# Performance work log

Hardware: AMD Instinct MI355X
Metric: run time of the kernel (lower is better)

## Reference

```python
import jax, jax.numpy as jnp
import numpy as np

DT = 1.0
V_LAMBDA = 1e-4
V_RIDGE = 1e-4


def third_order_D(Np):
    # [Np-3, Np] banded third-difference operator
    M = Np - 3
    r = jnp.arange(M)
    D = jnp.zeros((M, Np), dtype=jnp.float32)
    D = D.at[r, r].set(-1.0).at[r, r + 1].set(3.0).at[r, r + 2].set(-3.0).at[r, r + 3].set(1.0)
    return D


def setup_inputs() -> dict:
    key = jax.random.key(0)
    k1, k2, k3 = jax.random.split(key, 3)
    B, N = 8192, 64
    dxy = jax.random.normal(k1, (B, N, 2), dtype=jnp.float32)
    theta = jax.random.normal(k2, (B, N + 1), dtype=jnp.float32)
    v0 = jax.random.normal(k3, (B,), dtype=jnp.float32)
    return {"dxy": dxy, "theta": theta, "v0": v0}


def reference(dxy, theta, v0):
    B, N, _ = dxy.shape  # theta: [B, N+1]
    g = (2.0 / DT) * dxy                     # [B, N, 2]
    b = g.reshape(B, 2 * N)                  # interleaved (x, y) per step
    cos_t = jnp.cos(theta)
    sin_t = jnp.sin(theta)

    # Assemble banded data matrix A: [B, 2N, N+1]
    rows = jnp.arange(N)
    A = jnp.zeros((B, 2 * N, N + 1), dtype=dxy.dtype)
    A = A.at[:, 2 * rows, rows].set(cos_t[:, :-1])
    A = A.at[:, 2 * rows, rows + 1].set(cos_t[:, 1:])
    A = A.at[:, 2 * rows + 1, rows].set(sin_t[:, :-1])
    A = A.at[:, 2 * rows + 1, rows + 1].set(sin_t[:, 1:])
    # data weights w = 1 -> Aw == A

    ATA = jnp.einsum('bij,bik->bjk', A, A)           # [B, N+1, N+1]
    rhs = jnp.einsum('bij,bi->bj', A[:, :, 1:], b)   # [B, N]
    rhs = rhs - ATA[:, 1:, 0] * v0[:, None]

    # Smoothness prior: third-order difference, lam3 = v_lambda / dt^6
    D3 = third_order_D(N + 1)
    DTD = (V_LAMBDA / DT ** 6) * (D3.T @ D3)         # [N+1, N+1], shared across batch
    rhs = rhs - DTD[1:, 0] * v0[:, None]

    lhs = ATA[:, 1:, 1:] + DTD[1:, 1:] + V_RIDGE * jnp.eye(N, dtype=dxy.dtype)
    L = jnp.linalg.cholesky(lhs)
    y = jax.scipy.linalg.cho_solve((L, True), rhs[..., None])[..., 0]  # [B, N]
    return jnp.concatenate([v0[:, None], y], axis=-1)                  # [B, N+1]
```

## Files before the change

kernel.cpp:

```cpp
#include <hip/hip_runtime.h>
#include <math.h>

#define LAM3  1e-4f
#define RIDGE 1e-4f
#define NN    64
#define NP    65

__device__ __forceinline__ float d3_diag(int f) {
    if (f == 0 || f == 64) return 1.f;
    if (f == 1 || f == 63) return 10.f;
    if (f == 2 || f == 62) return 19.f;
    return 20.f;
}
__device__ __forceinline__ float d3_off1(int f) {
    if (f == 1 || f == 64) return -3.f;
    if (f == 2 || f == 63) return -12.f;
    return -15.f;
}
__device__ __forceinline__ float d3_off2(int f) {
    if (f == 2 || f == 64) return 3.f;
    return 6.f;
}

__global__ __launch_bounds__(64, 1) void alpamayo_banded_solve(
    const float* __restrict__ dxy,
    const float* __restrict__ theta,
    const float* __restrict__ v0,
    float* __restrict__ out,
    int B)
{
    __shared__ float thS[64 * NP];
    __shared__ float dxS[64 * 130];

    const int tid = threadIdx.x;
    const long b0 = (long)blockIdx.x * 64;
    const int b = (int)b0 + tid;

    {
        const float4* g = (const float4*)(theta + b0 * NP);
        float4* s4 = (float4*)thS;
        const long lim = (long)B * NP - b0 * NP;
        #pragma unroll
        for (int it = 0; it < 17; ++it) {
            const int k = it * 64 + tid;
            if (k < 1040 && 4 * k + 3 < lim) s4[k] = g[k];
        }
    }
    {
        const float4* g = (const float4*)(dxy + b0 * 2 * NN);
        const long lim4 = ((long)B * 2 * NN - b0 * 2 * NN) / 4;
        #pragma unroll
        for (int it = 0; it < 32; ++it) {
            const int k = it * 64 + tid;
            if (k < lim4) {
                const float4 q = g[k];
                const int flat = 4 * k;
                const int addr = flat + 2 * (flat >> 7);
                dxS[addr + 0] = q.x; dxS[addr + 1] = q.y;
                dxS[addr + 2] = q.z; dxS[addr + 3] = q.w;
            }
        }
    }
    const float v0b = (b < B) ? v0[b] : 0.f;
    __syncthreads();

    if (b < B) {
        const float* thL = thS + tid * NP;
        const float* dxL = dxS + tid * 130;

        float L1a[NN], L2a[NN], L3a[NN], rda[NN], z[NN];

        float sp, cp;
        __sincosf(thL[0], &sp, &cp);
        float bxp = dxL[0], byp = dxL[1];

        float p1L1 = 0.f, p1L2 = 0.f, p2L1 = 0.f;
        float rd1 = 0.f, rd2 = 0.f, rd3 = 0.f;
        float z1 = 0.f, z2 = 0.f, z3 = 0.f;

        #pragma unroll
        for (int i = 0; i < NN; ++i) {
            const int f = i + 1;
            float sf, cf;
            __sincosf(thL[f], &sf, &cf);
            const float e = cp * cf + sp * sf;

            float bxc = 0.f, byc = 0.f;
            if (f < NN) { bxc = dxL[2 * f]; byc = dxL[2 * f + 1]; }
            float rhs = 2.f * (cf * (bxp + bxc) + sf * (byp + byc));

            if (i == 0) rhs -= (e + LAM3 * -3.f) * v0b;
            if (i == 1) rhs -= (LAM3 *  3.f) * v0b;
            if (i == 2) rhs -= (LAM3 * -1.f) * v0b;

            const float a0 = (f == NN ? 1.f : 2.f) + LAM3 * d3_diag(f) + RIDGE;
            const float a1 = e + LAM3 * d3_off1(f);
            const float a2 = LAM3 * d3_off2(f);
            const float a3 = LAM3 * -1.f;

            const float Li3 = a3 * rd3;
            const float Li2 = (a2 - Li3 * p2L1) * rd2;
            const float Li1 = (a1 - Li3 * p1L2 - Li2 * p1L1) * rd1;
            const float dg  = a0 - Li3 * Li3 - Li2 * Li2 - Li1 * Li1;
            const float rd0 = __builtin_amdgcn_rsqf(dg);

            const float zi = (rhs - Li3 * z3 - Li2 * z2 - Li1 * z1) * rd0;

            L1a[i] = Li1; L2a[i] = Li2; L3a[i] = Li3; rda[i] = rd0; z[i] = zi;

            p2L1 = p1L1; p1L1 = Li1; p1L2 = Li2;
            rd3 = rd2; rd2 = rd1; rd1 = rd0;
            z3 = z2; z2 = z1; z1 = zi;
            cp = cf; sp = sf; bxp = bxc; byp = byc;
        }

        float* yL = thS + tid * NP;
        float y1 = 0.f, y2 = 0.f, y3 = 0.f;
        #pragma unroll
        for (int i = NN - 1; i >= 0; --i) {
            float yi = z[i];
            if (i + 1 < NN) yi -= L1a[i + 1] * y1;
            if (i + 2 < NN) yi -= L2a[i + 2] * y2;
            if (i + 3 < NN) yi -= L3a[i + 3] * y3;
            yi *= rda[i];
            yL[1 + i] = yi;
            y3 = y2; y2 = y1; y1 = yi;
        }
        yL[0] = v0b;
    }
    __syncthreads();

    {
        float4* g = (float4*)(out + b0 * NP);
        const float4* s4 = (const float4*)thS;
        const long lim = (long)B * NP - b0 * NP;
        #pragma unroll
        for (int it = 0; it < 17; ++it) {
            const int k = it * 64 + tid;
            if (k < 1040 && 4 * k + 3 < lim) g[k] = s4[k];
        }
    }
}

extern "C" void kernel_launch(void* const* d_in, const int* in_sizes, int n_in,
                              void* d_out, int out_size, void* d_ws, size_t ws_size,
                              hipStream_t stream) {
    const float* dxy   = (const float*)d_in[0];
    const float* theta = (const float*)d_in[1];
    const float* v0    = (const float*)d_in[2];
    float* out = (float*)d_out;
    const int B = in_sizes[2];
    const int blocks = (B + 63) / 64;
    alpamayo_banded_solve<<<blocks, 64, 0, stream>>>(dxy, theta, v0, out, B);
}
```

Before: 78.49 us.

## Split banded solve into parallel prep kernel and sequential Cholesky kernel

Splits the single kernel in two. A 256-thread prep kernel computes sin/cos, the off-diagonal terms and the right-hand side in parallel across four threads per batch row, and writes them to workspace in a transposed layout. A 64-thread solve kernel then reads these with coalesced loads and runs only the serial Cholesky recurrence. This takes the trig and data-shuffling work off the serial critical path of each thread, at the cost of an extra launch and a round trip of 2*64*B floats through global memory. Bounds checks for a partial last block are removed, so it assumes B is a multiple of 64.

```diff
diff --git a/kernel.cpp b/kernel.cpp
--- a/kernel.cpp
+++ b/kernel.cpp
@@ -22,123 +22,151 @@
     return 6.f;
 }
 
-__global__ __launch_bounds__(64, 1) void alpamayo_banded_solve(
+__global__ __launch_bounds__(256, 1) void alpamayo_prep(
     const float* __restrict__ dxy,
     const float* __restrict__ theta,
+    const float* __restrict__ v0,
+    float* __restrict__ eT,
+    float* __restrict__ rT,
+    int B)
+{
+    __shared__ __attribute__((aligned(16))) float thS[64 * NP];
+    __shared__ float cS[64 * NP];
+    __shared__ float sS[64 * NP];
+    __shared__ float bxS[64 * NP];
+    __shared__ float byS[64 * NP];
+
+    const int tid = threadIdx.x;
+    const int b0 = blockIdx.x * 64;
+
+    {
+        const float4* g = (const float4*)(theta + (long)b0 * NP);
+        float4* s4 = (float4*)thS;
+        #pragma unroll
+        for (int it = 0; it < 5; ++it) {
+            const int k = it * 256 + tid;
+            if (k < 1040) s4[k] = g[k];
+        }
+    }
+    {
+        const float4* g = (const float4*)(dxy + (long)b0 * 128);
+        #pragma unroll
+        for (int it = 0; it < 8; ++it) {
+            const int k = it * 256 + tid;
+            const float4 q = g[k];
+            const int flat = 4 * k;
+            const int bl = flat >> 7;
+            const int i  = (flat & 127) >> 1;
+            float* bx = bxS + bl * NP + i;
+            float* by = byS + bl * NP + i;
+            bx[0] = q.x; by[0] = q.y; bx[1] = q.z; by[1] = q.w;
+        }
+    }
+    if (tid < 64) { bxS[tid * NP + 64] = 0.f; byS[tid * NP + 64] = 0.f; }
+    __syncthreads();
+
+    #pragma unroll
+    for (int it = 0; it < 17; ++it) {
+        const int k = it * 256 + tid;
+        if (k < 4160) {
+            float sv, cv;
+            __sincosf(thS[k], &sv, &cv);
+            sS[k] = sv; cS[k] = cv;
+        }
+    }
+    __syncthreads();
+
+    const int bl = tid & 63;
+    const int qr = tid >> 6;
+    const int b  = b0 + bl;
+    const float* cL  = cS  + bl * NP;
+    const float* sL  = sS  + bl * NP;
+    const float* bxL = bxS + bl * NP;
+    const float* byL = byS + bl * NP;
+    const float v0b = v0[b];
+
+    #pragma unroll
+    for (int p = 0; p < 16; ++p) {
+        const int i = p * 4 + qr;
+        const int f = i + 1;
+        const float e   = cL[i] * cL[f] + sL[i] * sL[f];
+        float rhs = 2.f * (cL[f] * (bxL[i] + bxL[f]) + sL[f] * (byL[i] + byL[f]));
+        if (i == 0) rhs -= (e + LAM3 * -3.f) * v0b;
+        if (i == 1) rhs -= (LAM3 *  3.f) * v0b;
+        if (i == 2) rhs -= (LAM3 * -1.f) * v0b;
+        eT[i * B + b] = e;
+        rT[i * B + b] = rhs;
+    }
+}
+
+__global__ __launch_bounds__(64, 1) void alpamayo_solve(
+    const float* __restrict__ eT,
+    const float* __restrict__ rT,
     const float* __restrict__ v0,
     float* __restrict__ out,
     int B)
 {
-    __shared__ float thS[64 * NP];
-    __shared__ float dxS[64 * 130];
+    __shared__ __attribute__((aligned(16))) float yS[64 * NP];
 
     const int tid = threadIdx.x;
-    const long b0 = (long)blockIdx.x * 64;
-    const int b = (int)b0 + tid;
+    const int b0 = blockIdx.x * 64;
+    const int b  = b0 + tid;
 
-    {
-        const float4* g = (const float4*)(theta + b0 * NP);
-        float4* s4 = (float4*)thS;
-        const long lim = (long)B * NP - b0 * NP;
-        #pragma unroll
-        for (int it = 0; it < 17; ++it) {
-            const int k = it * 64 + tid;
-            if (k < 1040 && 4 * k + 3 < lim) s4[k] = g[k];
-        }
+    float L1a[NN], L2a[NN], L3a[NN], rda[NN], z[NN];
+
+    float p1L1 = 0.f, p1L2 = 0.f, p2L1 = 0.f;
+    float rd1 = 0.f, rd2 = 0.f, rd3 = 0.f;
+    float z1 = 0.f, z2 = 0.f, z3 = 0.f;
+
+    const float* ep = eT + b;
+    const float* rp = rT + b;
+
+    #pragma unroll
+    for (int i = 0; i < NN; ++i) {
+        const int f = i + 1;
+        const float e   = ep[i * B];
+        const float rhs = rp[i * B];
+
+        const float a0 = (f == NN ? 1.f : 2.f) + LAM3 * d3_diag(f) + RIDGE;
+        const float a1 = e + LAM3 * d3_off1(f);
+        const float a2 = LAM3 * d3_off2(f);
+        const float a3 = LAM3 * -1.f;
+
+        const float Li3 = a3 * rd3;
+        const float Li2 = (a2 - Li3 * p2L1) * rd2;
+        const float Li1 = (a1 - Li3 * p1L2 - Li2 * p1L1) * rd1;
+        const float dg  = a0 - Li3 * Li3 - Li2 * Li2 - Li1 * Li1;
+        const float rd0 = __builtin_amdgcn_rsqf(dg);
+        const float zi  = (rhs - Li3 * z3 - Li2 * z2 - Li1 * z1) * rd0;
+
+        L1a[i] = Li1; L2a[i] = Li2; L3a[i] = Li3; rda[i] = rd0; z[i] = zi;
+
+        p2L1 = p1L1; p1L1 = Li1; p1L2 = Li2;
+        rd3 = rd2; rd2 = rd1; rd1 = rd0;
+        z3 = z2; z2 = z1; z1 = zi;
     }
-    {
-        const float4* g = (const float4*)(dxy + b0 * 2 * NN);
-        const long lim4 = ((long)B * 2 * NN - b0 * 2 * NN) / 4;
-        #pragma unroll
-        for (int it = 0; it < 32; ++it) {
-            const int k = it * 64 + tid;
-            if (k < lim4) {
-                const float4 q = g[k];
-                const int flat = 4 * k;
-                const int addr = flat + 2 * (flat >> 7);
-                dxS[addr + 0] = q.x; dxS[addr + 1] = q.y;
-                dxS[addr + 2] = q.z; dxS[addr + 3] = q.w;
-            }
-        }
+
+    float* yL = yS + tid * NP;
+    float y1 = 0.f, y2 = 0.f, y3 = 0.f;
+    #pragma unroll
+    for (int i = NN - 1; i >= 0; --i) {
+        float yi = z[i];
+        if (i + 1 < NN) yi -= L1a[i + 1] * y1;
+        if (i + 2 < NN) yi -= L2a[i + 2] * y2;
+        if (i + 3 < NN) yi -= L3a[i + 3] * y3;
+        yi *= rda[i];
+        yL[1 + i] = yi;
+        y3 = y2; y2 = y1; y1 = yi;
     }
-    const float v0b = (b < B) ? v0[b] : 0.f;
+    yL[0] = v0[b];
     __syncthreads();
 
-    if (b < B) {
-        const float* thL = thS + tid * NP;
-        const float* dxL = dxS + tid * 130;
-
-        float L1a[NN], L2a[NN], L3a[NN], rda[NN], z[NN];
-
-        float sp, cp;
-        __sincosf(thL[0], &sp, &cp);
-        float bxp = dxL[0], byp = dxL[1];
-
-        float p1L1 = 0.f, p1L2 = 0.f, p2L1 = 0.f;
-        float rd1 = 0.f, rd2 = 0.f, rd3 = 0.f;
-        float z1 = 0.f, z2 = 0.f, z3 = 0.f;
-
-        #pragma unroll
-        for (int i = 0; i < NN; ++i) {
-            const int f = i + 1;
-            float sf, cf;
-            __sincosf(thL[f], &sf, &cf);
-            const float e = cp * cf + sp * sf;
-
-            float bxc = 0.f, byc = 0.f;
-            if (f < NN) { bxc = dxL[2 * f]; byc = dxL[2 * f + 1]; }
-            float rhs = 2.f * (cf * (bxp + bxc) + sf * (byp + byc));
-
-            if (i == 0) rhs -= (e + LAM3 * -3.f) * v0b;
-            if (i == 1) rhs -= (LAM3 *  3.f) * v0b;
-            if (i == 2) rhs -= (LAM3 * -1.f) * v0b;
-
-            const float a0 = (f == NN ? 1.f : 2.f) + LAM3 * d3_diag(f) + RIDGE;
-            const float a1 = e + LAM3 * d3_off1(f);
-            const float a2 = LAM3 * d3_off2(f);
-            const float a3 = LAM3 * -1.f;
-
-            const float Li3 = a3 * rd3;
-            const float Li2 = (a2 - Li3 * p2L1) * rd2;
-            const float Li1 = (a1 - Li3 * p1L2 - Li2 * p1L1) * rd1;
-            const float dg  = a0 - Li3 * Li3 - Li2 * Li2 - Li1 * Li1;
-            const float rd0 = __builtin_amdgcn_rsqf(dg);
-
-            const float zi = (rhs - Li3 * z3 - Li2 * z2 - Li1 * z1) * rd0;
-
-            L1a[i] = Li1; L2a[i] = Li2; L3a[i] = Li3; rda[i] = rd0; z[i] = zi;
-
-            p2L1 = p1L1; p1L1 = Li1; p1L2 = Li2;
-            rd3 = rd2; rd2 = rd1; rd1 = rd0;
-            z3 = z2; z2 = z1; z1 = zi;
-            cp = cf; sp = sf; bxp = bxc; byp = byc;
-        }
-
-        float* yL = thS + tid * NP;
-        float y1 = 0.f, y2 = 0.f, y3 = 0.f;
-        #pragma unroll
-        for (int i = NN - 1; i >= 0; --i) {
-            float yi = z[i];
-            if (i + 1 < NN) yi -= L1a[i + 1] * y1;
-            if (i + 2 < NN) yi -= L2a[i + 2] * y2;
-            if (i + 3 < NN) yi -= L3a[i + 3] * y3;
-            yi *= rda[i];
-            yL[1 + i] = yi;
-            y3 = y2; y2 = y1; y1 = yi;
-        }
-        yL[0] = v0b;
-    }
-    __syncthreads();
-
-    {
-        float4* g = (float4*)(out + b0 * NP);
-        const float4* s4 = (const float4*)thS;
-        const long lim = (long)B * NP - b0 * NP;
-        #pragma unroll
-        for (int it = 0; it < 17; ++it) {
-            const int k = it * 64 + tid;
-            if (k < 1040 && 4 * k + 3 < lim) g[k] = s4[k];
-        }
+    float4* go = (float4*)(out + (long)b0 * NP);
+    const float4* s4 = (const float4*)yS;
+    #pragma unroll
+    for (int it = 0; it < 17; ++it) {
+        const int k = it * 64 + tid;
+        if (k < 1040) go[k] = s4[k];
     }
 }
 
@@ -150,6 +178,11 @@
     const float* v0    = (const float*)d_in[2];
     float* out = (float*)d_out;
     const int B = in_sizes[2];
+
+    float* eT = (float*)d_ws;
+    float* rT = eT + (long)NN * B;
+
     const int blocks = (B + 63) / 64;
-    alpamayo_banded_solve<<<blocks, 64, 0, stream>>>(dxy, theta, v0, out, B);
+    alpamayo_prep <<<blocks, 256, 0, stream>>>(dxy, theta, v0, eT, rT, B);
+    alpamayo_solve<<<blocks,  64, 0, stream>>>(eT, rT, v0, out, B);
 }
```

Measured after the change: 68.30 us. 13.0% less time.
